# Performance work log

Measured on AMD Instinct MI355X. Metric: run time of the kernel, lower is better.

Reference implementation:

```python
import jax, jax.numpy as jnp
import numpy as np

B, T, C = 4, 2048, 1024
H, D = 16, 64


def setup_inputs() -> dict:
    key = jax.random.key(0)
    ks = jax.random.split(key, 6)
    s = 0.02
    return {
        "x": jax.random.normal(ks[0], (B, T, C), dtype=jnp.float32),
        "wq": jax.random.normal(ks[1], (H, C, D), dtype=jnp.float32) * s,
        "wk": jax.random.normal(ks[2], (H, C, D), dtype=jnp.float32) * s,
        "wv": jax.random.normal(ks[3], (H, C, D), dtype=jnp.float32) * s,
        "w_proj": jax.random.normal(ks[4], (C, C), dtype=jnp.float32) * s,
        "b_proj": jnp.zeros((C,), dtype=jnp.float32),
    }


def reference(x, wq, wk, wv, w_proj, b_proj):
    b, t, c = x.shape
    # per-head projections, vectorized over heads: [B,T,C] x [H,C,D] -> [B,H,T,D]
    q = jnp.einsum("btc,hcd->bhtd", x, wq)
    k = jnp.einsum("btc,hcd->bhtd", x, wk)
    v = jnp.einsum("btc,hcd->bhtd", x, wv)
    # NOTE: original scales by C**-0.5 where C = n_embd (not head_size)
    scale = jnp.asarray(c, x.dtype) ** -0.5
    scores = jnp.einsum("bhtd,bhsd->bhts", q, k) * scale  # [B,H,T,T]
    causal = jnp.tril(jnp.ones((t, t), dtype=bool))
    scores = jnp.where(causal, scores, jnp.finfo(x.dtype).min)
    wei = jax.nn.softmax(scores, axis=-1)
    out = jnp.einsum("bhts,bhsd->bhtd", wei, v)  # [B,H,T,D]
    out = out.transpose(0, 2, 1, 3).reshape(b, t, c)  # concat heads
    return out @ w_proj + b_proj
```

## Files before the change

kernel.cpp:

```cpp
#include <hip/hip_runtime.h>
#include <hip/hip_bf16.h>
#include <stdint.h>

#define B_ 4
#define T_ 2048
#define C_ 1024
#define H_ 16
#define D_ 64

typedef __attribute__((ext_vector_type(8))) short bf16x8;
typedef __attribute__((ext_vector_type(4))) short short4v;
typedef __attribute__((ext_vector_type(4))) float f32x4;

static __device__ __forceinline__ short f2bf(float f) {
    union { float f; unsigned u; } v; v.f = f;
    unsigned r = v.u + 0x7fffu + ((v.u >> 16) & 1u);
    return (short)(r >> 16);
}

static __device__ __forceinline__ float fast_exp2(float x) {
    float r;
    asm("v_exp_f32 %0, %1" : "=v"(r) : "v"(x));
    return r;
}

#define GLD_LDS16(g, l) __builtin_amdgcn_global_load_lds( \
    (const __attribute__((address_space(1))) void*)(g),   \
    (__attribute__((address_space(3))) void*)(l), 16, 0, 0)

#define QSCALE 0.04508422f

__global__ void pack_x(const float* __restrict__ x, short* __restrict__ xb) {
    int t = blockIdx.x * blockDim.x + threadIdx.x;
    const float* src = x + (size_t)t * 8;
    float4 v0 = *(const float4*)src;
    float4 v1 = *(const float4*)(src + 4);
    bf16x8 o;
    o[0] = f2bf(v0.x); o[1] = f2bf(v0.y); o[2] = f2bf(v0.z); o[3] = f2bf(v0.w);
    o[4] = f2bf(v1.x); o[5] = f2bf(v1.y); o[6] = f2bf(v1.z); o[7] = f2bf(v1.w);
    *(bf16x8*)(xb + (size_t)t * 8) = o;
}

__global__ void pack_wqkv2(const float* __restrict__ wq, const float* __restrict__ wk,
                           const float* __restrict__ wv, short* __restrict__ out) {
    __shared__ short tile[64][72];
    const int qh = blockIdx.y;
    const int qkv = qh >> 4, h = qh & 15;
    const int c0 = blockIdx.x * 64;
    const float* w = ((qkv == 0) ? wq : (qkv == 1) ? wk : wv) + (size_t)h * (C_ * D_);
    const int t = threadIdx.x;
    const int r = t >> 2;
    const int dc = (t & 3) * 16;

    const float* src = w + (size_t)(c0 + r) * D_ + dc;
#pragma unroll
    for (int j = 0; j < 4; ++j) {
        float4 v = *(const float4*)(src + j * 4);
        short4v s;
        s[0] = f2bf(v.x); s[1] = f2bf(v.y); s[2] = f2bf(v.z); s[3] = f2bf(v.w);
        *(short4v*)&tile[r][dc + j * 4] = s;
    }
    __syncthreads();

    const int d = t >> 2;
    const int cc = (t & 3) * 16;
    bf16x8 o0, o1;
#pragma unroll
    for (int j = 0; j < 8; ++j) {
        o0[j] = tile[cc + j][d];
        o1[j] = tile[cc + 8 + j][d];
    }
    short* dst = out + ((size_t)qkv * 1024 + h * 64 + d) * C_ + c0 + cc;
    *(bf16x8*)dst = o0;
    *(bf16x8*)(dst + 8) = o1;
}

__global__ void pack_wproj2(const float* __restrict__ wp, short* __restrict__ out) {
    __shared__ short tile[64][72];
    const int c0 = blockIdx.x * 64;
    const int n0 = blockIdx.y * 64;
    const int t = threadIdx.x;
    const int r = t >> 2;
    const int nc = (t & 3) * 16;

    const float* src = wp + (size_t)(c0 + r) * C_ + n0 + nc;
#pragma unroll
    for (int j = 0; j < 4; ++j) {
        float4 v = *(const float4*)(src + j * 4);
        short4v s;
        s[0] = f2bf(v.x); s[1] = f2bf(v.y); s[2] = f2bf(v.z); s[3] = f2bf(v.w);
        *(short4v*)&tile[r][nc + j * 4] = s;
    }
    __syncthreads();

    const int n = t >> 2;
    const int cc = (t & 3) * 16;
    bf16x8 o0, o1;
#pragma unroll
    for (int j = 0; j < 8; ++j) {
        o0[j] = tile[cc + j][n];
        o1[j] = tile[cc + 8 + j][n];
    }
    short* dst = out + (size_t)(n0 + n) * C_ + c0 + cc;
    *(bf16x8*)dst = o0;
    *(bf16x8*)(dst + 8) = o1;
}

template<int MODE>
__global__ __launch_bounds__(256)
void gemm_lds(const short* __restrict__ A, const short* __restrict__ Bt,
              void* __restrict__ Cptr, const float* __restrict__ bias,
              int M, int N, int K) {
    __shared__ short As[128 * 64];
    __shared__ short Bs[128 * 64];
    const int tid = threadIdx.x;
    const int lane = tid & 63, wid = tid >> 6;
    const int wr = wid >> 1, wc = wid & 1;
    const int l15 = lane & 15, l4 = lane >> 4;
    const int m0 = blockIdx.y * 128, n0 = blockIdx.x * 128;

    f32x4 acc[4][4] = {};

    for (int k0 = 0; k0 < K; k0 += 64) {
#pragma unroll
        for (int p = 0; p < 4; ++p) {
            int e = p * 256 + tid;
            int r = e >> 3, pc = e & 7;
            int lc = pc ^ (r & 7);
            GLD_LDS16(A  + (size_t)(m0 + r) * K + k0 + lc * 8, As + e * 8);
            GLD_LDS16(Bt + (size_t)(n0 + r) * K + k0 + lc * 8, Bs + e * 8);
        }
        __syncthreads();

#pragma unroll
        for (int kk = 0; kk < 2; ++kk) {
            bf16x8 af[4], bfr[4];
#pragma unroll
            for (int m = 0; m < 4; ++m) {
                int row = wr * 64 + m * 16 + l15;
                int pc = (kk * 4 + l4) ^ (row & 7);
                af[m] = *(const bf16x8*)(As + row * 64 + pc * 8);
            }
#pragma unroll
            for (int n = 0; n < 4; ++n) {
                int row = wc * 64 + n * 16 + l15;
                int pc = (kk * 4 + l4) ^ (row & 7);
                bfr[n] = *(const bf16x8*)(Bs + row * 64 + pc * 8);
            }
#pragma unroll
            for (int m = 0; m < 4; ++m)
#pragma unroll
                for (int n = 0; n < 4; ++n)
                    acc[m][n] = __builtin_amdgcn_mfma_f32_16x16x32_bf16(af[m], bfr[n], acc[m][n], 0, 0, 0);
        }
        __syncthreads();
    }

#pragma unroll
    for (int m = 0; m < 4; ++m) {
        int row_base = m0 + wr * 64 + m * 16 + l4 * 4;
#pragma unroll
        for (int n = 0; n < 4; ++n) {
            int col = n0 + wc * 64 + n * 16 + l15;
#pragma unroll
            for (int r = 0; r < 4; ++r) {
                int row = row_base + r;
                float v = acc[m][n][r];
                if (MODE == 1) {
                    ((float*)Cptr)[(size_t)row * N + col] = v + bias[col];
                } else {
                    if (col < 1024) v *= QSCALE;
                    ((short*)Cptr)[(size_t)row * N + col] = f2bf(v);
                }
            }
        }
    }
}

__device__ __forceinline__ void softmax_phase(
    f32x4 S[4], f32x4 O[4], float* mrow, float* srow,
    int qrow0, int s0, bool diag, int l15, int l4, short* ps) {
    float pmax[4];
#pragma unroll
    for (int r = 0; r < 4; ++r) pmax[r] = -1e30f;
#pragma unroll
    for (int n = 0; n < 4; ++n) {
#pragma unroll
        for (int r = 0; r < 4; ++r) {
            float v = S[n][r];
            if (diag) {
                int scol = s0 + n * 16 + l15;
                if (scol > qrow0 + r) v = -1e30f;
            }
            S[n][r] = v;
            pmax[r] = fmaxf(pmax[r], v);
        }
    }
#pragma unroll
    for (int r = 0; r < 4; ++r) {
        float v = pmax[r];
        v = fmaxf(v, __shfl_xor(v, 1));
        v = fmaxf(v, __shfl_xor(v, 2));
        v = fmaxf(v, __shfl_xor(v, 4));
        v = fmaxf(v, __shfl_xor(v, 8));
        pmax[r] = v;
    }
    int ok = (pmax[0] <= mrow[0] + 8.0f) & (pmax[1] <= mrow[1] + 8.0f) &
             (pmax[2] <= mrow[2] + 8.0f) & (pmax[3] <= mrow[3] + 8.0f);
    if (!__all(ok)) {
#pragma unroll
        for (int r = 0; r < 4; ++r) {
            float mnew = fmaxf(mrow[r], pmax[r]);
            float fr = fast_exp2(mrow[r] - mnew);
            mrow[r] = mnew;
            srow[r] *= fr;
#pragma unroll
            for (int n = 0; n < 4; ++n) O[n][r] *= fr;
        }
    }
    float psum[4];
#pragma unroll
    for (int r = 0; r < 4; ++r) psum[r] = 0.0f;
#pragma unroll
    for (int n = 0; n < 4; ++n) {
#pragma unroll
        for (int r = 0; r < 4; ++r) {
            float p = fast_exp2(S[n][r] - mrow[r]);
            psum[r] += p;
            ps[(l4 * 4 + r) * 72 + n * 16 + l15] = f2bf(p);
        }
    }
#pragma unroll
    for (int r = 0; r < 4; ++r) {
        float v = psum[r];
        v += __shfl_xor(v, 1);
        v += __shfl_xor(v, 2);
        v += __shfl_xor(v, 4);
        v += __shfl_xor(v, 8);
        srow[r] += v;
    }
}

__global__ __launch_bounds__(256)
void attn_v14(const short* __restrict__ qkv, short* __restrict__ out) {
    const int pi = blockIdx.x;
    const int bh = blockIdx.y;
    const int b = bh >> 4;
    const int h = bh & 15;
    const int qA0 = pi * 64;
    const int qB0 = (31 - pi) * 64;
    const int ntA = pi + 1;
    const int ntB = 32 - pi;
    const int tid = threadIdx.x;
    const int wave = tid >> 6;
    const int lane = tid & 63;
    const int l15 = lane & 15, l4 = lane >> 4;

    __shared__ short Vt[2][64][72];
    __shared__ short Ps[4][2][16][72];

    const size_t rs = 3 * C_;
    const short* qbA = qkv + ((size_t)b * T_ + qA0) * rs + h * 64;
    const short* qbB = qkv + ((size_t)b * T_ + qB0) * rs + h * 64;
    const short* kb  = qkv + (size_t)b * T_ * rs + C_ + h * 64;
    const short* vb  = qkv + (size_t)b * T_ * rs + 2 * C_ + h * 64;

    bf16x8 aqA0 = *(const bf16x8*)(qbA + (size_t)(wave * 16 + l15) * rs + l4 * 8);
    bf16x8 aqA1 = *(const bf16x8*)(qbA + (size_t)(wave * 16 + l15) * rs + 32 + l4 * 8);
    bf16x8 aqB0 = *(const bf16x8*)(qbB + (size_t)(wave * 16 + l15) * rs + l4 * 8);
    bf16x8 aqB1 = *(const bf16x8*)(qbB + (size_t)(wave * 16 + l15) * rs + 32 + l4 * 8);

    f32x4 OA[4] = {}, OB[4] = {};
    float mA[4], sA[4], mB[4], sB[4];
#pragma unroll
    for (int r = 0; r < 4; ++r) { mA[r] = mB[r] = -1e30f; sA[r] = sB[r] = 0.0f; }

    short* psB = &Ps[wave][0][0][0];
    short* psA = &Ps[wave][1][0][0];
    const int qrB = qB0 + wave * 16 + l4 * 4;
    const int qrA = qA0 + wave * 16 + l4 * 4;

    auto qk_sm = [&](int s0, bool actA) {
        bf16x8 bk0[4], bk1[4];
#pragma unroll
        for (int n = 0; n < 4; ++n) {
            const short* kr = kb + (size_t)(s0 + n * 16 + l15) * rs;
            bk0[n] = *(const bf16x8*)(kr + l4 * 8);
            bk1[n] = *(const bf16x8*)(kr + 32 + l4 * 8);
        }
        f32x4 S[4];
#pragma unroll
        for (int n = 0; n < 4; ++n) {
            f32x4 z = {};
            z = __builtin_amdgcn_mfma_f32_16x16x32_bf16(aqB0, bk0[n], z, 0, 0, 0);
            S[n] = __builtin_amdgcn_mfma_f32_16x16x32_bf16(aqB1, bk1[n], z, 0, 0, 0);
        }
        softmax_phase(S, OB, mB, sB, qrB, s0, s0 == qB0, l15, l4, psB);
        if (actA) {
            f32x4 SA[4];
#pragma unroll
            for (int n = 0; n < 4; ++n) {
                f32x4 z = {};
                z = __builtin_amdgcn_mfma_f32_16x16x32_bf16(aqA0, bk0[n], z, 0, 0, 0);
                SA[n] = __builtin_amdgcn_mfma_f32_16x16x32_bf16(aqA1, bk1[n], z, 0, 0, 0);
            }
            softmax_phase(SA, OA, mA, sA, qrA, s0, s0 == qA0, l15, l4, psA);
        }
    };

    auto pv = [&](int slot, bool actA) {
        bf16x8 apB0 = *(const bf16x8*)(psB + l15 * 72 + l4 * 8);
        bf16x8 apB1 = *(const bf16x8*)(psB + l15 * 72 + 32 + l4 * 8);
#pragma unroll
        for (int n = 0; n < 4; ++n) {
            bf16x8 bv0 = *(const bf16x8*)&Vt[slot][n * 16 + l15][l4 * 8];
            bf16x8 bv1 = *(const bf16x8*)&Vt[slot][n * 16 + l15][32 + l4 * 8];
            OB[n] = __builtin_amdgcn_mfma_f32_16x16x32_bf16(apB0, bv0, OB[n], 0, 0, 0);
            OB[n] = __builtin_amdgcn_mfma_f32_16x16x32_bf16(apB1, bv1, OB[n], 0, 0, 0);
        }
        if (actA) {
            bf16x8 apA0 = *(const bf16x8*)(psA + l15 * 72 + l4 * 8);
            bf16x8 apA1 = *(const bf16x8*)(psA + l15 * 72 + 32 + l4 * 8);
#pragma unroll
            for (int n = 0; n < 4; ++n) {
                bf16x8 bv0 = *(const bf16x8*)&Vt[slot][n * 16 + l15][l4 * 8];
                bf16x8 bv1 = *(const bf16x8*)&Vt[slot][n * 16 + l15][32 + l4 * 8];
                OA[n] = __builtin_amdgcn_mfma_f32_16x16x32_bf16(apA0, bv0, OA[n], 0, 0, 0);
                OA[n] = __builtin_amdgcn_mfma_f32_16x16x32_bf16(apA1, bv1, OA[n], 0, 0, 0);
            }
        }
    };

    const int npair = ntB & ~1;
    for (int t = 0; t < npair; t += 2) {
        const int s0 = t * 64;
        __syncthreads();

#pragma unroll
        for (int p = 0; p < 2; ++p) {
            int e = p * 256 + tid;
            int d = e & 63, sc = e >> 6;
            bf16x8 v0, v1;
#pragma unroll
            for (int j = 0; j < 8; ++j) {
                v0[j] = vb[(size_t)(s0 + sc * 8 + j) * rs + d];
                v1[j] = vb[(size_t)(s0 + 64 + sc * 8 + j) * rs + d];
            }
            *(bf16x8*)&Vt[0][d][sc * 8] = v0;
            *(bf16x8*)&Vt[1][d][sc * 8] = v1;
        }

        qk_sm(s0, t < ntA);

        __syncthreads();

        pv(0, t < ntA);
        qk_sm(s0 + 64, t + 1 < ntA);

        asm volatile("s_waitcnt lgkmcnt(0)" ::: "memory");
        __builtin_amdgcn_sched_barrier(0);

        pv(1, t + 1 < ntA);
    }

    if (ntB & 1) {
        const int s0 = npair * 64;
        __syncthreads();
#pragma unroll
        for (int p = 0; p < 2; ++p) {
            int e = p * 256 + tid;
            int d = e & 63, sc = e >> 6;
            bf16x8 v0;
#pragma unroll
            for (int j = 0; j < 8; ++j)
                v0[j] = vb[(size_t)(s0 + sc * 8 + j) * rs + d];
            *(bf16x8*)&Vt[0][d][sc * 8] = v0;
        }
        qk_sm(s0, npair < ntA);
        __syncthreads();
        pv(0, npair < ntA);
    }

#pragma unroll
    for (int r = 0; r < 4; ++r) {
        int rowB = qB0 + wave * 16 + l4 * 4 + r;
        int rowA = qA0 + wave * 16 + l4 * 4 + r;
        float invB = 1.0f / sB[r];
        float invA = 1.0f / sA[r];
        size_t obB = ((size_t)b * T_ + rowB) * C_ + h * 64;
        size_t obA = ((size_t)b * T_ + rowA) * C_ + h * 64;
#pragma unroll
        for (int n = 0; n < 4; ++n) {
            out[obB + n * 16 + l15] = f2bf(OB[n][r] * invB);
            out[obA + n * 16 + l15] = f2bf(OA[n][r] * invA);
        }
    }
}

extern "C" void kernel_launch(void* const* d_in, const int* in_sizes, int n_in,
                              void* d_out, int out_size, void* d_ws, size_t ws_size,
                              hipStream_t stream) {
    const float* x     = (const float*)d_in[0];
    const float* wq    = (const float*)d_in[1];
    const float* wk    = (const float*)d_in[2];
    const float* wv    = (const float*)d_in[3];
    const float* wproj = (const float*)d_in[4];
    const float* bproj = (const float*)d_in[5];
    float* out = (float*)d_out;

    short* wqkv_t  = (short*)d_ws;
    short* wproj_t = wqkv_t + 3072 * 1024;
    short* qkv_b   = wproj_t + 1024 * 1024;
    short* attn_b  = qkv_b + (size_t)8192 * 3072;
    short* xb      = attn_b;

    pack_x<<<4096, 256, 0, stream>>>(x, xb);
    pack_wqkv2<<<dim3(16, 48), 256, 0, stream>>>(wq, wk, wv, wqkv_t);
    pack_wproj2<<<dim3(16, 16), 256, 0, stream>>>(wproj, wproj_t);

    gemm_lds<2><<<dim3(24, 64), 256, 0, stream>>>(
        xb, wqkv_t, qkv_b, nullptr, 8192, 3072, 1024);

    attn_v14<<<dim3(16, 64), 256, 0, stream>>>(qkv_b, attn_b);

    gemm_lds<1><<<dim3(8, 64), 256, 0, stream>>>(
        attn_b, wproj_t, out, bproj, 8192, 1024, 1024);
}
```

Baseline: 276.4 us.

## Write V transposed from QKV GEMM epilogue and stage it via async LDS loads

The QKV projection GEMM now writes Q and K into a packed 2048-wide buffer and writes V already transposed (per batch, head and dim, along time) into a separate buffer. The attention kernel then stages V tiles with direct global-to-LDS 16-byte loads in an XOR-swizzled layout, replacing the per-element strided gather and in-register transpose. This removes many scattered 2-byte global loads in attention. In exchange, the GEMM epilogue does strided 8-byte transposed stores for V and the LDS read path adds swizzle arithmetic.

Measured after the change: 271.3 us. Within noise of the previous version (-1.9%).

```diff
diff --git a/kernel.cpp b/kernel.cpp
--- a/kernel.cpp
+++ b/kernel.cpp
@@ -109,8 +109,8 @@
 template<int MODE>
 __global__ __launch_bounds__(256)
 void gemm_lds(const short* __restrict__ A, const short* __restrict__ Bt,
-              void* __restrict__ Cptr, const float* __restrict__ bias,
-              int M, int N, int K) {
+              void* __restrict__ Cptr, short* __restrict__ vtptr,
+              const float* __restrict__ bias, int M, int N, int K) {
     __shared__ short As[128 * 64];
     __shared__ short Bs[128 * 64];
     const int tid = threadIdx.x;
@@ -162,15 +162,25 @@
 #pragma unroll
         for (int n = 0; n < 4; ++n) {
             int col = n0 + wc * 64 + n * 16 + l15;
-#pragma unroll
-            for (int r = 0; r < 4; ++r) {
-                int row = row_base + r;
-                float v = acc[m][n][r];
-                if (MODE == 1) {
-                    ((float*)Cptr)[(size_t)row * N + col] = v + bias[col];
+            if (MODE == 1) {
+#pragma unroll
+                for (int r = 0; r < 4; ++r)
+                    ((float*)Cptr)[(size_t)(row_base + r) * N + col] =
+                        acc[m][n][r] + bias[col];
+            } else {
+                if (col < 2048) {
+                    float q = (col < 1024) ? QSCALE : 1.0f;
+#pragma unroll
+                    for (int r = 0; r < 4; ++r)
+                        ((short*)Cptr)[(size_t)(row_base + r) * 2048 + col] =
+                            f2bf(acc[m][n][r] * q);
                 } else {
-                    if (col < 1024) v *= QSCALE;
-                    ((short*)Cptr)[(size_t)row * N + col] = f2bf(v);
+                    int cm = col - 2048;
+                    int bq = row_base >> 11, t = row_base & 2047;
+                    short4v s;
+                    s[0] = f2bf(acc[m][n][0]); s[1] = f2bf(acc[m][n][1]);
+                    s[2] = f2bf(acc[m][n][2]); s[3] = f2bf(acc[m][n][3]);
+                    *(short4v*)(vtptr + ((size_t)bq * 1024 + cm) * 2048 + t) = s;
                 }
             }
         }
@@ -242,7 +252,8 @@
 }
 
 __global__ __launch_bounds__(256)
-void attn_v14(const short* __restrict__ qkv, short* __restrict__ out) {
+void attn_v16(const short* __restrict__ qk, const short* __restrict__ vt,
+              short* __restrict__ out) {
     const int pi = blockIdx.x;
     const int bh = blockIdx.y;
     const int b = bh >> 4;
@@ -256,14 +267,14 @@
     const int lane = tid & 63;
     const int l15 = lane & 15, l4 = lane >> 4;
 
-    __shared__ short Vt[2][64][72];
+    __shared__ short Vt[2][64][64];
     __shared__ short Ps[4][2][16][72];
 
-    const size_t rs = 3 * C_;
-    const short* qbA = qkv + ((size_t)b * T_ + qA0) * rs + h * 64;
-    const short* qbB = qkv + ((size_t)b * T_ + qB0) * rs + h * 64;
-    const short* kb  = qkv + (size_t)b * T_ * rs + C_ + h * 64;
-    const short* vb  = qkv + (size_t)b * T_ * rs + 2 * C_ + h * 64;
+    const size_t rs = 2 * C_;
+    const short* qbA = qk + ((size_t)b * T_ + qA0) * rs + h * 64;
+    const short* qbB = qk + ((size_t)b * T_ + qB0) * rs + h * 64;
+    const short* kb  = qk + (size_t)b * T_ * rs + 1024 + h * 64;
+    const short* vtb = vt + (size_t)bh * 64 * T_;
 
     bf16x8 aqA0 = *(const bf16x8*)(qbA + (size_t)(wave * 16 + l15) * rs + l4 * 8);
     bf16x8 aqA1 = *(const bf16x8*)(qbA + (size_t)(wave * 16 + l15) * rs + 32 + l4 * 8);
@@ -280,6 +291,20 @@
     const int qrB = qB0 + wave * 16 + l4 * 4;
     const int qrA = qA0 + wave * 16 + l4 * 4;
 
+    const int sr = tid >> 3;
+    const int spc = tid & 7;
+
+    auto stage = [&](int slot, int s0) {
+#pragma unroll
+        for (int p = 0; p < 2; ++p) {
+            int e = p * 256 + tid;
+            int r = (p == 0) ? sr : (sr + 32);
+            int lc = spc ^ (r & 7);
+            GLD_LDS16(vtb + (size_t)r * T_ + s0 + lc * 8,
+                      &Vt[slot][0][0] + e * 8);
+        }
+    };
+
     auto qk_sm = [&](int s0, bool actA) {
         bf16x8 bk0[4], bk1[4];
 #pragma unroll
@@ -311,10 +336,12 @@
     auto pv = [&](int slot, bool actA) {
         bf16x8 apB0 = *(const bf16x8*)(psB + l15 * 72 + l4 * 8);
         bf16x8 apB1 = *(const bf16x8*)(psB + l15 * 72 + 32 + l4 * 8);
+        const int x7 = l15 & 7;
 #pragma unroll
         for (int n = 0; n < 4; ++n) {
-            bf16x8 bv0 = *(const bf16x8*)&Vt[slot][n * 16 + l15][l4 * 8];
-            bf16x8 bv1 = *(const bf16x8*)&Vt[slot][n * 16 + l15][32 + l4 * 8];
+            const short* vrow = &Vt[slot][n * 16 + l15][0];
+            bf16x8 bv0 = *(const bf16x8*)(vrow + ((l4 ^ x7) * 8));
+            bf16x8 bv1 = *(const bf16x8*)(vrow + (((l4 + 4) ^ x7) * 8));
             OB[n] = __builtin_amdgcn_mfma_f32_16x16x32_bf16(apB0, bv0, OB[n], 0, 0, 0);
             OB[n] = __builtin_amdgcn_mfma_f32_16x16x32_bf16(apB1, bv1, OB[n], 0, 0, 0);
         }
@@ -323,8 +350,9 @@
             bf16x8 apA1 = *(const bf16x8*)(psA + l15 * 72 + 32 + l4 * 8);
 #pragma unroll
             for (int n = 0; n < 4; ++n) {
-                bf16x8 bv0 = *(const bf16x8*)&Vt[slot][n * 16 + l15][l4 * 8];
-                bf16x8 bv1 = *(const bf16x8*)&Vt[slot][n * 16 + l15][32 + l4 * 8];
+                const short* vrow = &Vt[slot][n * 16 + l15][0];
+                bf16x8 bv0 = *(const bf16x8*)(vrow + ((l4 ^ x7) * 8));
+                bf16x8 bv1 = *(const bf16x8*)(vrow + (((l4 + 4) ^ x7) * 8));
                 OA[n] = __builtin_amdgcn_mfma_f32_16x16x32_bf16(apA0, bv0, OA[n], 0, 0, 0);
                 OA[n] = __builtin_amdgcn_mfma_f32_16x16x32_bf16(apA1, bv1, OA[n], 0, 0, 0);
             }
@@ -336,19 +364,8 @@
         const int s0 = t * 64;
         __syncthreads();
 
-#pragma unroll
-        for (int p = 0; p < 2; ++p) {
-            int e = p * 256 + tid;
-            int d = e & 63, sc = e >> 6;
-            bf16x8 v0, v1;
-#pragma unroll
-            for (int j = 0; j < 8; ++j) {
-                v0[j] = vb[(size_t)(s0 + sc * 8 + j) * rs + d];
-                v1[j] = vb[(size_t)(s0 + 64 + sc * 8 + j) * rs + d];
-            }
-            *(bf16x8*)&Vt[0][d][sc * 8] = v0;
-            *(bf16x8*)&Vt[1][d][sc * 8] = v1;
-        }
+        stage(0, s0);
+        stage(1, s0 + 64);
 
         qk_sm(s0, t < ntA);
 
@@ -366,16 +383,7 @@
     if (ntB & 1) {
         const int s0 = npair * 64;
         __syncthreads();
-#pragma unroll
-        for (int p = 0; p < 2; ++p) {
-            int e = p * 256 + tid;
-            int d = e & 63, sc = e >> 6;
-            bf16x8 v0;
-#pragma unroll
-            for (int j = 0; j < 8; ++j)
-                v0[j] = vb[(size_t)(s0 + sc * 8 + j) * rs + d];
-            *(bf16x8*)&Vt[0][d][sc * 8] = v0;
-        }
+        stage(0, s0);
         qk_sm(s0, npair < ntA);
         __syncthreads();
         pv(0, npair < ntA);
@@ -410,8 +418,9 @@
 
     short* wqkv_t  = (short*)d_ws;
     short* wproj_t = wqkv_t + 3072 * 1024;
-    short* qkv_b   = wproj_t + 1024 * 1024;
-    short* attn_b  = qkv_b + (size_t)8192 * 3072;
+    short* qk_b    = wproj_t + 1024 * 1024;
+    short* vt_b    = qk_b + (size_t)8192 * 2048;
+    short* attn_b  = vt_b + (size_t)64 * 64 * 2048;
     short* xb      = attn_b;
 
     pack_x<<<4096, 256, 0, stream>>>(x, xb);
@@ -419,10 +428,10 @@
     pack_wproj2<<<dim3(16, 16), 256, 0, stream>>>(wproj, wproj_t);
 
     gemm_lds<2><<<dim3(24, 64), 256, 0, stream>>>(
-        xb, wqkv_t, qkv_b, nullptr, 8192, 3072, 1024);
-
-    attn_v14<<<dim3(16, 64), 256, 0, stream>>>(qkv_b, attn_b);
+        xb, wqkv_t, qk_b, vt_b, nullptr, 8192, 3072, 1024);
+
+    attn_v16<<<dim3(16, 64), 256, 0, stream>>>(qk_b, vt_b, attn_b);
 
     gemm_lds<1><<<dim3(8, 64), 256, 0, stream>>>(
-        attn_b, wproj_t, out, bproj, 8192, 1024, 1024);
-}
+        attn_b, wproj_t, out, nullptr, bproj, 8192, 1024, 1024);
+}
```
